# Kernel optimization log

Measured on AMD Instinct MI355X. Metric: run time of the kernel, lower is better.

The kernel has to match this reference:

```python
import jax, jax.numpy as jnp
import numpy as np

NUM_LAYERS = 2
D_MODEL = 64
D_INNER = 128   # expand * d_model
D_STATE = 128   # min(2*input_size, 256)
DT_RANK = 4     # ceil(d_model / 16)
D_CONV = 4
HIDDEN = 64


def _causal_dwconv(x, w, b):
    # x: [B, L, C], w: [C, K], b: [C]  -- causal depthwise conv (left pad K-1)
    K = w.shape[1]
    L = x.shape[1]
    xp = jnp.pad(x, ((0, 0), (K - 1, 0), (0, 0)))
    y = sum(xp[:, k:k + L, :] * w[:, k][None, None, :] for k in range(K))
    return y + b


def _selective_scan(u, delta, A, B, C, Dp):
    # u, delta: [b,L,d]; A: [d,n]; B, C: [b,L,n]; Dp: [d]
    dA = jnp.exp(jnp.einsum('bld,dn->lbdn', delta, A))          # [L,b,d,n]
    dBu = jnp.einsum('bld,bln,bld->lbdn', delta, B, u)           # [L,b,d,n]
    Ct = jnp.swapaxes(C, 0, 1)                                   # [L,b,n]

    def step(h, inp):
        dA_t, dBu_t, C_t = inp
        h = dA_t * h + dBu_t                                     # [b,d,n]
        y = jnp.einsum('bdn,bn->bd', h, C_t)
        return h, y

    h0 = jnp.zeros(dA.shape[1:], dA.dtype)
    _, ys = jax.lax.scan(step, h0, (dA, dBu, Ct))                # ys: [L,b,d]
    return jnp.swapaxes(ys, 0, 1) + u * Dp


def _mamba_layer(x, in_w, conv_w, conv_b, xproj_w, dt_w, dt_b, A_log, Dp, out_w):
    xz = x @ in_w.T                                              # [B,L,2*d_inner]
    xi, z = jnp.split(xz, 2, axis=-1)
    xi = jax.nn.silu(_causal_dwconv(xi, conv_w, conv_b))
    xdbl = xi @ xproj_w.T                                        # [B,L,dt_rank+2*d_state]
    delta = jax.nn.softplus(xdbl[..., :DT_RANK] @ dt_w.T + dt_b)
    Bm = xdbl[..., DT_RANK:DT_RANK + D_STATE]
    Cm = xdbl[..., DT_RANK + D_STATE:]
    A = -jnp.exp(A_log)
    y = _selective_scan(xi, delta, A, Bm, Cm, Dp)
    y = y * jax.nn.silu(z)
    return y @ out_w.T


def setup_inputs() -> dict:
    key = jax.random.key(0)
    ks = jax.random.split(key, 10)
    B, L = 4, 1024
    s = 0.05
    x = jax.random.normal(ks[0], (B, L, D_MODEL), dtype=jnp.float32)
    in_proj_w = jax.random.normal(ks[1], (NUM_LAYERS, 2 * D_INNER, D_MODEL)) * s
    conv_w = jax.random.normal(ks[2], (NUM_LAYERS, D_INNER, D_CONV)) * 0.2
    conv_b = jax.random.normal(ks[3], (NUM_LAYERS, D_INNER)) * 0.02
    x_proj_w = jax.random.normal(ks[4], (NUM_LAYERS, DT_RANK + 2 * D_STATE, D_INNER)) * s
    dt_w = jax.random.normal(ks[5], (NUM_LAYERS, D_INNER, DT_RANK)) * 0.1
    dt_b = jnp.full((NUM_LAYERS, D_INNER), -4.6, dtype=jnp.float32)  # softplus -> ~0.01
    # S4D-real init: A_log = log(1..d_state)
    A_log = jnp.log(jnp.broadcast_to(
        jnp.arange(1, D_STATE + 1, dtype=jnp.float32), (NUM_LAYERS, D_INNER, D_STATE)))
    D = jnp.ones((NUM_LAYERS, D_INNER), dtype=jnp.float32)
    out_proj_w = jax.random.normal(ks[6], (NUM_LAYERS, D_MODEL, D_INNER)) * s
    fc_w = jax.random.normal(ks[7], (HIDDEN, D_MODEL)) * s
    fc_b = jax.random.normal(ks[8], (HIDDEN,)) * 0.02
    return {"x": x, "in_proj_w": in_proj_w, "conv_w": conv_w, "conv_b": conv_b,
            "x_proj_w": x_proj_w, "dt_w": dt_w, "dt_b": dt_b, "A_log": A_log,
            "D": D, "out_proj_w": out_proj_w, "fc_w": fc_w, "fc_b": fc_b}


def reference(x, in_proj_w, conv_w, conv_b, x_proj_w, dt_w, dt_b, A_log, D, out_proj_w, fc_w, fc_b):
    h = x
    for l in range(NUM_LAYERS):
        h = _mamba_layer(h, in_proj_w[l], conv_w[l], conv_b[l], x_proj_w[l],
                         dt_w[l], dt_b[l], A_log[l], D[l], out_proj_w[l])
    return h @ fc_w.T + fc_b
```

## Files before the change

### kernel.cpp

```cpp
#include <hip/hip_runtime.h>
#include <hip/hip_bf16.h>

#define BB 4
#define LL 1024
#define DM 64
#define DI 128
#define DS 128
#define DTR 4
#define KC 4
#define RT 8
#define GRP 8
#define CS 128
#define NC 8
#define L2E 1.44269504f

#define XWT_OFF   0
#define INWT_OFF  65536
#define OWT_OFF   98304
#define CWT_OFF   114688
#define CB_OFF    115712
#define DTWT_OFF  115968
#define DTB_OFF   116992
#define XWDT_OFF  117248

__device__ __forceinline__ float bf2f(__hip_bfloat16 v) { return __bfloat162float(v); }
__device__ __forceinline__ float silu_f(float x) { return x / (1.f + __expf(-x)); }

__device__ __forceinline__ float ldf(const void* p, long i, unsigned bf) {
    return bf ? __bfloat162float(((const __hip_bfloat16*)p)[i]) : ((const float*)p)[i];
}

__device__ __forceinline__ void fma4(float4& acc, float s, const float4 w) {
    acc.x = fmaf(s, w.x, acc.x); acc.y = fmaf(s, w.y, acc.y);
    acc.z = fmaf(s, w.z, acc.z); acc.w = fmaf(s, w.w, acc.w);
}

__device__ __forceinline__ int permrb(int j) { return (j & 31) * 16 + (j >> 5); }

__device__ __forceinline__ void probe_flags(const void* dtb, const void* fcw,
                                            unsigned& bfe, unsigned& bfw) {
    unsigned w = *(const unsigned*)dtb;
    bfe = (w == 0xC093C093u) ? 1u : 0u;
    const unsigned* p = (const unsigned*)fcw;
    int cnt = 0;
    for (int i = 0; i < 32; ++i) {
        unsigned m = p[i] & 0x7FFFu;
        if (m >= 0x3000u && m < 0x4200u) cnt++;
    }
    bfw = (cnt >= 28) ? 1u : 0u;
}

__global__ __launch_bounds__(256) void k_prep(
        const void* __restrict__ inw, const void* __restrict__ xw,
        const void* __restrict__ ow, const void* __restrict__ cw,
        const void* __restrict__ cb, const void* __restrict__ dtw,
        const void* __restrict__ dtb, const void* __restrict__ fcw,
        unsigned* __restrict__ flags, float* __restrict__ WT) {
    unsigned bfe, bfw;
    probe_flags(dtb, fcw, bfe, bfw);
    int bid = blockIdx.x, tid = threadIdx.x;
    if (bid < 28) {
        const void* src; long soff; int srcK; float* dst; int dstN; int n0, k0;
        if (bid < 16) {
            int l = bid >> 3, kt = (bid >> 2) & 1, nt = bid & 3;
            src = xw; srcK = 128; soff = (long)l * 260 * 128 + 4 * 128;
            n0 = nt * 64; k0 = kt * 64; dst = WT + XWT_OFF + l * 32768; dstN = 256;
        } else if (bid < 24) {
            int b2 = bid - 16, l = b2 >> 2, nt = b2 & 3;
            src = inw; srcK = 64; soff = (long)l * 256 * 64;
            n0 = nt * 64; k0 = 0; dst = WT + INWT_OFF + l * 16384; dstN = 256;
        } else {
            int b2 = bid - 24, l = b2 >> 1, kt = b2 & 1;
            src = ow; srcK = 128; soff = (long)l * 64 * 128;
            n0 = 0; k0 = kt * 64; dst = WT + OWT_OFF + l * 8192; dstN = 64;
        }
        __shared__ float tile[64 * 65];
        for (int i = tid; i < 4096; i += 256) {
            int ln = i >> 6, lk = i & 63;
            tile[ln * 65 + lk] = ldf(src, soff + (long)(n0 + ln) * srcK + k0 + lk, bfw);
        }
        __syncthreads();
        for (int i = tid; i < 4096; i += 256) {
            int lk = i >> 6, ln = i & 63;
            dst[(long)(k0 + lk) * dstN + n0 + ln] = tile[ln * 65 + lk];
        }
    } else {
        if (tid == 0) { flags[0] = bfe; flags[1] = bfw; flags[2] = bfe & bfw; }
        for (int j = tid; j < 1024; j += 256) {
            int l = j >> 9, t = (j >> 7) & 3, d = j & 127;
            WT[CWT_OFF + j] = ldf(cw, (long)l * 512 + d * 4 + t, bfw);
        }
        for (int j = tid; j < 256; j += 256) WT[CB_OFF + j] = ldf(cb, j, bfw);
        for (int j = tid; j < 1024; j += 256) {
            int l = j >> 9, r = (j >> 7) & 3, d = j & 127;
            WT[DTWT_OFF + j] = ldf(dtw, (long)l * 512 + d * 4 + r, bfw);
        }
        for (int j = tid; j < 256; j += 256) WT[DTB_OFF + j] = ldf(dtb, j, bfe);
        for (int j = tid; j < 1024; j += 256) {
            int l = j >> 9, rem = j & 511;
            WT[XWDT_OFF + j] = ldf(xw, (long)l * 260 * 128 + rem, bfw);
        }
    }
}

__global__ __launch_bounds__(256) void k_inproj(
        const void* __restrict__ xin,
        const float* __restrict__ wt, const unsigned* __restrict__ flags,
        float* __restrict__ xzx, float* __restrict__ sz) {
    unsigned bfx = flags[0];
    int row0 = permrb(blockIdx.x) * RT;
    int tid = threadIdx.x, lane = tid & 63, g = tid >> 6;
    __shared__ float act[RT * DM];
    for (int i = tid; i < RT * DM; i += 256)
        act[i] = ldf(xin, (long)(row0 + (i >> 6)) * DM + (i & 63), bfx);
    __syncthreads();
    const float4* wt4 = (const float4*)wt;
    float4 acc[2];
    acc[0] = make_float4(0.f, 0.f, 0.f, 0.f);
    acc[1] = make_float4(0.f, 0.f, 0.f, 0.f);
#pragma unroll 8
    for (int k4 = 0; k4 < DM / 4; ++k4) {
        float4 w0 = wt4[(k4 * 4 + 0) * 64 + lane];
        float4 w1 = wt4[(k4 * 4 + 1) * 64 + lane];
        float4 w2 = wt4[(k4 * 4 + 2) * 64 + lane];
        float4 w3 = wt4[(k4 * 4 + 3) * 64 + lane];
#pragma unroll
        for (int r = 0; r < 2; ++r) {
            float4 av = *(const float4*)&act[(g * 2 + r) * DM + k4 * 4];
            fma4(acc[r], av.x, w0); fma4(acc[r], av.y, w1);
            fma4(acc[r], av.z, w2); fma4(acc[r], av.w, w3);
        }
    }
    int n0 = lane * 4;
#pragma unroll
    for (int r = 0; r < 2; ++r) {
        int row = row0 + g * 2 + r;
        if (n0 < DI) {
            *(float4*)&xzx[(size_t)row * DI + n0] = acc[r];
        } else {
            float4 v;
            v.x = silu_f(acc[r].x); v.y = silu_f(acc[r].y);
            v.z = silu_f(acc[r].z); v.w = silu_f(acc[r].w);
            *(float4*)&sz[(size_t)row * DI + (n0 - DI)] = v;
        }
    }
}

__global__ __launch_bounds__(256) void k_xproj(
        const float* __restrict__ xzx,
        const float* __restrict__ cwT, const float* __restrict__ cbF,
        const float* __restrict__ xwT, const float* __restrict__ xwdtF,
        const float* __restrict__ dtwT, const float* __restrict__ dtbF,
        float* __restrict__ xiw, float* __restrict__ dlt,
        float* __restrict__ Bm, float* __restrict__ Cm) {
    int row0 = permrb(blockIdx.x) * RT;
    int b = row0 >> 10, l0 = row0 & (LL - 1);
    int tid = threadIdx.x, lane = tid & 63, g = tid >> 6;
    __shared__ float xc[(RT + KC - 1) * DI];
    __shared__ float act[RT * DI];
    __shared__ float dtp[RT * DTR];
    for (int i = tid; i < (RT + KC - 1) * DI; i += 256) {
        int r = (i >> 7) - (KC - 1);
        int l = l0 + r;
        xc[i] = (l >= 0) ? xzx[((size_t)b * LL + l) * DI + (i & 127)] : 0.f;
    }
    __syncthreads();
    for (int i = tid; i < RT * DI; i += 256) {
        int r = i >> 7, d = i & 127;
        float a = cbF[d];
#pragma unroll
        for (int t = 0; t < KC; ++t) a = fmaf(xc[(r + t) * DI + d], cwT[t * DI + d], a);
        float v = silu_f(a);
        act[i] = v;
        xiw[(size_t)(row0 + r) * DI + d] = v;
    }
    __syncthreads();
    const float4* wt4 = (const float4*)xwT;
    float4 acc[2];
    acc[0] = make_float4(0.f, 0.f, 0.f, 0.f);
    acc[1] = make_float4(0.f, 0.f, 0.f, 0.f);
#pragma unroll 8
    for (int k4 = 0; k4 < DI / 4; ++k4) {
        float4 w0 = wt4[(k4 * 4 + 0) * 64 + lane];
        float4 w1 = wt4[(k4 * 4 + 1) * 64 + lane];
        float4 w2 = wt4[(k4 * 4 + 2) * 64 + lane];
        float4 w3 = wt4[(k4 * 4 + 3) * 64 + lane];
#pragma unroll
        for (int r = 0; r < 2; ++r) {
            float4 av = *(const float4*)&act[(g * 2 + r) * DI + k4 * 4];
            fma4(acc[r], av.x, w0); fma4(acc[r], av.y, w1);
            fma4(acc[r], av.z, w2); fma4(acc[r], av.w, w3);
        }
    }
    int n0 = lane * 4;
#pragma unroll
    for (int r = 0; r < 2; ++r) {
        int row = row0 + g * 2 + r;
        if (n0 < DS) *(float4*)&Bm[(size_t)row * DS + n0] = acc[r];
        else         *(float4*)&Cm[(size_t)row * DS + (n0 - DS)] = acc[r];
    }
    if (tid < RT * DTR) {
        int r = tid >> 2, i = tid & 3;
        float a = 0.f;
#pragma unroll
        for (int k4 = 0; k4 < DI / 4; ++k4) {
            float4 av = *(const float4*)&act[r * DI + k4 * 4];
            float4 wv = *(const float4*)&xwdtF[i * DI + k4 * 4];
            a = fmaf(av.x, wv.x, a); a = fmaf(av.y, wv.y, a);
            a = fmaf(av.z, wv.z, a); a = fmaf(av.w, wv.w, a);
        }
        dtp[tid] = a;
    }
    __syncthreads();
    if (tid < DI) {
        float dw0 = dtwT[0 * DI + tid], dw1 = dtwT[1 * DI + tid];
        float dw2 = dtwT[2 * DI + tid], dw3 = dtwT[3 * DI + tid];
        float bv = dtbF[tid];
#pragma unroll
        for (int r = 0; r < RT; ++r) {
            float a = bv;
            a = fmaf(dtp[r * 4 + 0], dw0, a);
            a = fmaf(dtp[r * 4 + 1], dw1, a);
            a = fmaf(dtp[r * 4 + 2], dw2, a);
            a = fmaf(dtp[r * 4 + 3], dw3, a);
            dlt[(size_t)(row0 + r) * DI + tid] = (a > 20.f) ? a : log1pf(__expf(a));
        }
    }
}

__global__ __launch_bounds__(256) void k_scanA(
        const float* __restrict__ dlt, const float* __restrict__ xiw,
        const float* __restrict__ Bm,
        const void* __restrict__ Alog, long aoff,
        const unsigned* __restrict__ flags,
        float* __restrict__ hend, float* __restrict__ S) {
    __shared__ float dsh[CS * 4];
    __shared__ float ush[CS * 4];
    int gid = blockIdx.x;
    int dg = gid / (BB * NC);
    int bc = gid % (BB * NC);
    int b = bc / NC, c = bc % NC;
    int d0 = dg * 4;
    int tid = threadIdx.x;
    int w = tid >> 6, t = tid & 63;
    int d = d0 + w;
    int c0 = c * CS;
    unsigned bfe = flags[0];
    float A0 = -L2E * __expf(ldf(Alog, aoff + (long)d * DS + 2 * t, bfe));
    float A1 = -L2E * __expf(ldf(Alog, aoff + (long)d * DS + 2 * t + 1, bfe));
    for (int i = tid; i < CS * 4; i += 256) {
        size_t src = ((size_t)b * LL + c0 + (i >> 2)) * DI + d0 + (i & 3);
        dsh[i] = dlt[src];
        ush[i] = xiw[src];
    }
    __syncthreads();
    const float2* Bg = (const float2*)(Bm + ((size_t)b * LL + c0) * DS) + t;
    float h0 = 0.f, h1v = 0.f, sumd = 0.f;
    for (int li = 0; li < CS; li += GRP) {
        float dl[GRP], ul[GRP], ea0[GRP], ea1[GRP];
        float2 Bv[GRP];
#pragma unroll
        for (int s = 0; s < GRP; ++s) {
            dl[s] = dsh[(li + s) * 4 + w];
            ul[s] = ush[(li + s) * 4 + w];
            Bv[s] = Bg[(size_t)(li + s) * (DS / 2)];
        }
#pragma unroll
        for (int s = 0; s < GRP; ++s) {
            ea0[s] = exp2f(dl[s] * A0);
            ea1[s] = exp2f(dl[s] * A1);
        }
#pragma unroll
        for (int s = 0; s < GRP; ++s) {
            float db = dl[s] * ul[s];
            h0  = fmaf(ea0[s], h0,  db * Bv[s].x);
            h1v = fmaf(ea1[s], h1v, db * Bv[s].y);
            sumd += dl[s];
        }
    }
    size_t hbase = (((size_t)b * DI + d) * NC + c) * DS;
    ((float2*)(hend + hbase))[t] = make_float2(h0, h1v);
    if (t == 0) S[((size_t)b * DI + d) * NC + c] = sumd;
}

__global__ __launch_bounds__(256) void k_scanC(
        const float* __restrict__ dlt, const float* __restrict__ xiw,
        const float* __restrict__ Bm, const float* __restrict__ Cm,
        const void* __restrict__ Alog, long aoff,
        const void* __restrict__ Dp, long doff,
        const unsigned* __restrict__ flags,
        const float* __restrict__ hend, const float* __restrict__ S,
        float* __restrict__ y) {
    __shared__ float dsh[CS * 4];
    __shared__ float ush[CS * 4];
    __shared__ float ysh[CS * 4];
    __shared__ float Wred[4 * 520];
    int gid = blockIdx.x;
    int dg = gid / (BB * NC);
    int bc = gid % (BB * NC);
    int b = bc / NC, c = bc % NC;
    int d0 = dg * 4;
    int tid = threadIdx.x;
    int w = tid >> 6, t = tid & 63;
    int d = d0 + w;
    int c0 = c * CS;
    unsigned bfe = flags[0];
    float A0 = -L2E * __expf(ldf(Alog, aoff + (long)d * DS + 2 * t, bfe));
    float A1 = -L2E * __expf(ldf(Alog, aoff + (long)d * DS + 2 * t + 1, bfe));
    float Dv = ldf(Dp, doff + d, bfe);
    for (int i = tid; i < CS * 4; i += 256) {
        size_t src = ((size_t)b * LL + c0 + (i >> 2)) * DI + d0 + (i & 3);
        dsh[i] = dlt[src];
        ush[i] = xiw[src];
    }
    __syncthreads();
    float h0 = 0.f, h1v = 0.f;
    const float2* hep = (const float2*)(hend + (((size_t)b * DI + d) * NC) * DS);
    const float* Sp = S + ((size_t)b * DI + d) * NC;
    for (int cc = 0; cc < c; ++cc) {
        float2 he = hep[(size_t)cc * (DS / 2) + t];
        float s = Sp[cc];
        h0  = fmaf(exp2f(A0 * s), h0,  he.x);
        h1v = fmaf(exp2f(A1 * s), h1v, he.y);
    }
    const float2* Bg = (const float2*)(Bm + ((size_t)b * LL + c0) * DS) + t;
    const float2* Cg = (const float2*)(Cm + ((size_t)b * LL + c0) * DS) + t;
    float* Wl = Wred + w * 520;
    int rbase = (t >> 3) * 65 + (t & 7) * 8;
    for (int li = 0; li < CS; li += GRP) {
        float dl[GRP], ul[GRP], ea0[GRP], ea1[GRP], cv[GRP];
        float2 Bv[GRP], Cv[GRP];
#pragma unroll
        for (int s = 0; s < GRP; ++s) {
            dl[s] = dsh[(li + s) * 4 + w];
            ul[s] = ush[(li + s) * 4 + w];
            Bv[s] = Bg[(size_t)(li + s) * (DS / 2)];
            Cv[s] = Cg[(size_t)(li + s) * (DS / 2)];
        }
#pragma unroll
        for (int s = 0; s < GRP; ++s) {
            ea0[s] = exp2f(dl[s] * A0);
            ea1[s] = exp2f(dl[s] * A1);
        }
#pragma unroll
        for (int s = 0; s < GRP; ++s) {
            float db = dl[s] * ul[s];
            h0  = fmaf(ea0[s], h0,  db * Bv[s].x);
            h1v = fmaf(ea1[s], h1v, db * Bv[s].y);
            cv[s] = fmaf(h0, Cv[s].x, h1v * Cv[s].y);
        }
#pragma unroll
        for (int s = 0; s < GRP; ++s) Wl[s * 65 + t] = cv[s];
        float pt = 0.f;
#pragma unroll
        for (int j = 0; j < 8; ++j) pt += Wl[rbase + j];
        pt += __shfl_xor(pt, 1, 64);
        pt += __shfl_xor(pt, 2, 64);
        pt += __shfl_xor(pt, 4, 64);
        if ((t & 7) == 0) {
            int l = li + (t >> 3);
            ysh[l * 4 + w] = pt + ush[l * 4 + w] * Dv;
        }
    }
    __syncthreads();
    for (int i = tid; i < CS * 4; i += 256)
        y[((size_t)b * LL + c0 + (i >> 2)) * DI + d0 + (i & 3)] = ysh[i];
}

__global__ __launch_bounds__(256) void k_mid(
        const float* __restrict__ y, float* __restrict__ sz,
        const float* __restrict__ owT, const float* __restrict__ inwT,
        float* __restrict__ xzx) {
    int row0 = permrb(blockIdx.x) * RT;
    int tid = threadIdx.x, lane = tid & 63, g = tid >> 6;
    __shared__ float act[RT * DI];
    __shared__ float hsh[RT * DM];
    for (int i = tid; i < RT * DI; i += 256) {
        size_t idx = (size_t)(row0 + (i >> 7)) * DI + (i & 127);
        act[i] = y[idx] * sz[idx];
    }
    __syncthreads();
    {
        float acc[2] = {0.f, 0.f};
#pragma unroll 8
        for (int k4 = 0; k4 < DI / 4; ++k4) {
            float w0 = owT[(k4 * 4 + 0) * DM + lane];
            float w1 = owT[(k4 * 4 + 1) * DM + lane];
            float w2 = owT[(k4 * 4 + 2) * DM + lane];
            float w3 = owT[(k4 * 4 + 3) * DM + lane];
#pragma unroll
            for (int r = 0; r < 2; ++r) {
                float4 av = *(const float4*)&act[(g * 2 + r) * DI + k4 * 4];
                acc[r] = fmaf(av.x, w0, acc[r]); acc[r] = fmaf(av.y, w1, acc[r]);
                acc[r] = fmaf(av.z, w2, acc[r]); acc[r] = fmaf(av.w, w3, acc[r]);
            }
        }
#pragma unroll
        for (int r = 0; r < 2; ++r) hsh[(g * 2 + r) * DM + lane] = acc[r];
    }
    __syncthreads();
    {
        const float4* wt4 = (const float4*)inwT;
        float4 acc[2];
        acc[0] = make_float4(0.f, 0.f, 0.f, 0.f);
        acc[1] = make_float4(0.f, 0.f, 0.f, 0.f);
#pragma unroll 8
        for (int k4 = 0; k4 < DM / 4; ++k4) {
            float4 w0 = wt4[(k4 * 4 + 0) * 64 + lane];
            float4 w1 = wt4[(k4 * 4 + 1) * 64 + lane];
            float4 w2 = wt4[(k4 * 4 + 2) * 64 + lane];
            float4 w3 = wt4[(k4 * 4 + 3) * 64 + lane];
#pragma unroll
            for (int r = 0; r < 2; ++r) {
                float4 av = *(const float4*)&hsh[(g * 2 + r) * DM + k4 * 4];
                fma4(acc[r], av.x, w0); fma4(acc[r], av.y, w1);
                fma4(acc[r], av.z, w2); fma4(acc[r], av.w, w3);
            }
        }
        int n0 = lane * 4;
#pragma unroll
        for (int r = 0; r < 2; ++r) {
            int row = row0 + g * 2 + r;
            if (n0 < DI) {
                *(float4*)&xzx[(size_t)row * DI + n0] = acc[r];
            } else {
                float4 v;
                v.x = silu_f(acc[r].x); v.y = silu_f(acc[r].y);
                v.z = silu_f(acc[r].z); v.w = silu_f(acc[r].w);
                *(float4*)&sz[(size_t)row * DI + (n0 - DI)] = v;
            }
        }
    }
}

__global__ __launch_bounds__(256) void k_back(
        const float* __restrict__ y, const float* __restrict__ sz,
        const void* __restrict__ ow, long owoff,
        const void* __restrict__ fw, const void* __restrict__ fb,
        const unsigned* __restrict__ flags, void* __restrict__ out) {
    unsigned bfw = flags[1], obf = flags[2];
    int row0 = permrb(blockIdx.x) * RT;
    int tid = threadIdx.x, n = tid & 63, g = tid >> 6;
    __shared__ float owsh[DI * 65];
    __shared__ float fwsh[DM * 65];
    __shared__ float act[RT * DI];
    __shared__ float hsh[RT * DM];
    for (int i = tid; i < DM * DI; i += 256) {
        int nn = i >> 7, k = i & 127;
        owsh[k * 65 + nn] = ldf(ow, owoff + i, bfw);
    }
    for (int i = tid; i < DM * DM; i += 256) {
        int nn = i >> 6, k = i & 63;
        fwsh[k * 65 + nn] = ldf(fw, i, bfw);
    }
    for (int i = tid; i < RT * DI; i += 256) {
        size_t idx = (size_t)(row0 + (i >> 7)) * DI + (i & 127);
        act[i] = y[idx] * sz[idx];
    }
    __syncthreads();
    {
        float acc[2] = {0.f, 0.f};
#pragma unroll 8
        for (int k4 = 0; k4 < DI / 4; ++k4) {
            float w0 = owsh[(k4 * 4 + 0) * 65 + n];
            float w1 = owsh[(k4 * 4 + 1) * 65 + n];
            float w2 = owsh[(k4 * 4 + 2) * 65 + n];
            float w3 = owsh[(k4 * 4 + 3) * 65 + n];
#pragma unroll
            for (int r = 0; r < 2; ++r) {
                float4 av = *(const float4*)&act[(g * 2 + r) * DI + k4 * 4];
                acc[r] = fmaf(av.x, w0, acc[r]); acc[r] = fmaf(av.y, w1, acc[r]);
                acc[r] = fmaf(av.z, w2, acc[r]); acc[r] = fmaf(av.w, w3, acc[r]);
            }
        }
#pragma unroll
        for (int r = 0; r < 2; ++r) hsh[(g * 2 + r) * DM + n] = acc[r];
    }
    __syncthreads();
    {
        float bv = ldf(fb, n, bfw);
        float acc[2] = {bv, bv};
#pragma unroll 8
        for (int k4 = 0; k4 < DM / 4; ++k4) {
            float w0 = fwsh[(k4 * 4 + 0) * 65 + n];
            float w1 = fwsh[(k4 * 4 + 1) * 65 + n];
            float w2 = fwsh[(k4 * 4 + 2) * 65 + n];
            float w3 = fwsh[(k4 * 4 + 3) * 65 + n];
#pragma unroll
            for (int r = 0; r < 2; ++r) {
                float4 av = *(const float4*)&hsh[(g * 2 + r) * DM + k4 * 4];
                acc[r] = fmaf(av.x, w0, acc[r]); acc[r] = fmaf(av.y, w1, acc[r]);
                acc[r] = fmaf(av.z, w2, acc[r]); acc[r] = fmaf(av.w, w3, acc[r]);
            }
        }
#pragma unroll
        for (int r = 0; r < 2; ++r) {
            size_t idx = (size_t)(row0 + g * 2 + r) * DM + n;
            if (obf) ((__hip_bfloat16*)out)[idx] = __float2bfloat16(acc[r]);
            else     ((float*)out)[idx] = acc[r];
        }
    }
}

extern "C" void kernel_launch(void* const* d_in, const int* in_sizes, int n_in,
                              void* d_out, int out_size, void* d_ws, size_t ws_size,
                              hipStream_t stream) {
    const void* x    = d_in[0];
    const void* inw  = d_in[1];
    const void* cw   = d_in[2];
    const void* cb   = d_in[3];
    const void* xw   = d_in[4];
    const void* dtw  = d_in[5];
    const void* dtb  = d_in[6];
    const void* Alog = d_in[7];
    const void* Dp   = d_in[8];
    const void* ow   = d_in[9];
    const void* fcw  = d_in[10];
    const void* fcb  = d_in[11];

    const size_t NBL = (size_t)BB * LL;
    const int GB = (int)(NBL / RT);
    unsigned* flags = (unsigned*)d_ws;
    float* base = (float*)d_ws + 64;
    float* sz   = base;
    float* xiw  = sz + 524288;
    float* dlt  = xiw + 524288;
    float* Bmw  = dlt + 524288;
    float* Cmw  = Bmw + 524288;
    float* yw   = Cmw + 524288;
    float* hend = yw + 524288;
    float* S    = hend + 524288;
    float* xzx  = S + 4096;
    float* WT   = (float*)d_out;

    k_prep<<<29, 256, 0, stream>>>(inw, xw, ow, cw, cb, dtw, dtb, fcw, flags, WT);

    k_inproj<<<GB, 256, 0, stream>>>(x, WT + INWT_OFF, flags, xzx, sz);
    k_xproj<<<GB, 256, 0, stream>>>(xzx,
                                    WT + CWT_OFF, WT + CB_OFF,
                                    WT + XWT_OFF, WT + XWDT_OFF,
                                    WT + DTWT_OFF, WT + DTB_OFF,
                                    xiw, dlt, Bmw, Cmw);
    k_scanA<<<32 * BB * NC, 256, 0, stream>>>(dlt, xiw, Bmw, Alog, 0, flags, hend, S);
    k_scanC<<<32 * BB * NC, 256, 0, stream>>>(dlt, xiw, Bmw, Cmw, Alog, 0,
                                              Dp, 0, flags, hend, S, yw);
    k_mid<<<GB, 256, 0, stream>>>(yw, sz, WT + OWT_OFF, WT + INWT_OFF + 16384, xzx);
    k_xproj<<<GB, 256, 0, stream>>>(xzx,
                                    WT + CWT_OFF + 512, WT + CB_OFF + 128,
                                    WT + XWT_OFF + 32768, WT + XWDT_OFF + 512,
                                    WT + DTWT_OFF + 512, WT + DTB_OFF + 128,
                                    xiw, dlt, Bmw, Cmw);
    k_scanA<<<32 * BB * NC, 256, 0, stream>>>(dlt, xiw, Bmw, Alog, (long)DI * DS, flags, hend, S);
    k_scanC<<<32 * BB * NC, 256, 0, stream>>>(dlt, xiw, Bmw, Cmw, Alog, (long)DI * DS,
                                              Dp, DI, flags, hend, S, yw);
    k_back<<<GB, 256, 0, stream>>>(yw, sz, ow, (long)DM * DI, fcw, fcb, flags, d_out);
}
```

Measured before the change: 299.1 us.

## Fuse chunked scan passes into one kernel with inter-block flag handoff

Merges the two-pass chunked selective scan (chunk-end state pass, then output pass) into one kernel. Each block scans its chunk from a zero state, publishes its end state and delta sum, then waits on release/acquire flags from earlier chunks. It adds their carried-in contribution using a prefix sum of delta over the chunk. This removes one kernel launch and the duplicate recomputation of the local recurrence per layer. The price is spin-waiting that assumes earlier chunks' blocks are resident or already done, plus an extra exp pass for the carry term.

```diff
diff --git a/kernel.cpp b/kernel.cpp
--- a/kernel.cpp
+++ b/kernel.cpp
@@ -228,14 +228,20 @@
     }
 }
 
-__global__ __launch_bounds__(256) void k_scanA(
+__global__ __launch_bounds__(256) void k_scanF2(
         const float* __restrict__ dlt, const float* __restrict__ xiw,
-        const float* __restrict__ Bm,
+        const float* __restrict__ Bm, const float* __restrict__ Cm,
         const void* __restrict__ Alog, long aoff,
+        const void* __restrict__ Dp, long doff,
         const unsigned* __restrict__ flags,
-        float* __restrict__ hend, float* __restrict__ S) {
+        float* __restrict__ hend, float* __restrict__ S,
+        unsigned* __restrict__ flagArr, unsigned magic,
+        float* __restrict__ y) {
     __shared__ float dsh[CS * 4];
-    __shared__ float ush[CS * 4];
+    __shared__ float dush[CS * 4];
+    __shared__ float cdsh[CS * 4];
+    __shared__ float ysh[CS * 4];
+    __shared__ float Wred[4 * 520];
     int gid = blockIdx.x;
     int dg = gid / (BB * NC);
     int bc = gid % (BB * NC);
@@ -250,90 +256,43 @@
     float A1 = -L2E * __expf(ldf(Alog, aoff + (long)d * DS + 2 * t + 1, bfe));
     for (int i = tid; i < CS * 4; i += 256) {
         size_t src = ((size_t)b * LL + c0 + (i >> 2)) * DI + d0 + (i & 3);
-        dsh[i] = dlt[src];
-        ush[i] = xiw[src];
-    }
-    __syncthreads();
-    const float2* Bg = (const float2*)(Bm + ((size_t)b * LL + c0) * DS) + t;
-    float h0 = 0.f, h1v = 0.f, sumd = 0.f;
-    for (int li = 0; li < CS; li += GRP) {
-        float dl[GRP], ul[GRP], ea0[GRP], ea1[GRP];
-        float2 Bv[GRP];
-#pragma unroll
-        for (int s = 0; s < GRP; ++s) {
-            dl[s] = dsh[(li + s) * 4 + w];
-            ul[s] = ush[(li + s) * 4 + w];
-            Bv[s] = Bg[(size_t)(li + s) * (DS / 2)];
-        }
-#pragma unroll
-        for (int s = 0; s < GRP; ++s) {
-            ea0[s] = exp2f(dl[s] * A0);
-            ea1[s] = exp2f(dl[s] * A1);
-        }
-#pragma unroll
-        for (int s = 0; s < GRP; ++s) {
-            float db = dl[s] * ul[s];
-            h0  = fmaf(ea0[s], h0,  db * Bv[s].x);
-            h1v = fmaf(ea1[s], h1v, db * Bv[s].y);
-            sumd += dl[s];
-        }
-    }
-    size_t hbase = (((size_t)b * DI + d) * NC + c) * DS;
-    ((float2*)(hend + hbase))[t] = make_float2(h0, h1v);
-    if (t == 0) S[((size_t)b * DI + d) * NC + c] = sumd;
-}
-
-__global__ __launch_bounds__(256) void k_scanC(
-        const float* __restrict__ dlt, const float* __restrict__ xiw,
-        const float* __restrict__ Bm, const float* __restrict__ Cm,
-        const void* __restrict__ Alog, long aoff,
-        const void* __restrict__ Dp, long doff,
-        const unsigned* __restrict__ flags,
-        const float* __restrict__ hend, const float* __restrict__ S,
-        float* __restrict__ y) {
-    __shared__ float dsh[CS * 4];
-    __shared__ float ush[CS * 4];
-    __shared__ float ysh[CS * 4];
-    __shared__ float Wred[4 * 520];
-    int gid = blockIdx.x;
-    int dg = gid / (BB * NC);
-    int bc = gid % (BB * NC);
-    int b = bc / NC, c = bc % NC;
-    int d0 = dg * 4;
-    int tid = threadIdx.x;
-    int w = tid >> 6, t = tid & 63;
-    int d = d0 + w;
-    int c0 = c * CS;
-    unsigned bfe = flags[0];
-    float A0 = -L2E * __expf(ldf(Alog, aoff + (long)d * DS + 2 * t, bfe));
-    float A1 = -L2E * __expf(ldf(Alog, aoff + (long)d * DS + 2 * t + 1, bfe));
-    float Dv = ldf(Dp, doff + d, bfe);
-    for (int i = tid; i < CS * 4; i += 256) {
-        size_t src = ((size_t)b * LL + c0 + (i >> 2)) * DI + d0 + (i & 3);
-        dsh[i] = dlt[src];
-        ush[i] = xiw[src];
-    }
-    __syncthreads();
-    float h0 = 0.f, h1v = 0.f;
-    const float2* hep = (const float2*)(hend + (((size_t)b * DI + d) * NC) * DS);
-    const float* Sp = S + ((size_t)b * DI + d) * NC;
-    for (int cc = 0; cc < c; ++cc) {
-        float2 he = hep[(size_t)cc * (DS / 2) + t];
-        float s = Sp[cc];
-        h0  = fmaf(exp2f(A0 * s), h0,  he.x);
-        h1v = fmaf(exp2f(A1 * s), h1v, he.y);
+        float dl = dlt[src];
+        float ul = xiw[src];
+        dsh[i] = dl;
+        dush[i] = dl * ul;
+        ysh[i] = ul * ldf(Dp, doff + d0 + (i & 3), bfe);
+    }
+    __syncthreads();
+    {
+        float a = dsh[t * 4 + w];
+        float bb2 = dsh[(64 + t) * 4 + w];
+#pragma unroll
+        for (int off = 1; off < 64; off <<= 1) {
+            float n = __shfl(a, t - off, 64);
+            if (t >= off) a += n;
+        }
+        float T1 = __shfl(a, 63, 64);
+#pragma unroll
+        for (int off = 1; off < 64; off <<= 1) {
+            float n = __shfl(bb2, t - off, 64);
+            if (t >= off) bb2 += n;
+        }
+        bb2 += T1;
+        cdsh[t * 4 + w] = a;
+        cdsh[(64 + t) * 4 + w] = bb2;
     }
     const float2* Bg = (const float2*)(Bm + ((size_t)b * LL + c0) * DS) + t;
     const float2* Cg = (const float2*)(Cm + ((size_t)b * LL + c0) * DS) + t;
     float* Wl = Wred + w * 520;
     int rbase = (t >> 3) * 65 + (t & 7) * 8;
+    float h0 = 0.f, h1v = 0.f;
     for (int li = 0; li < CS; li += GRP) {
-        float dl[GRP], ul[GRP], ea0[GRP], ea1[GRP], cv[GRP];
+        float dl[GRP], du[GRP], ea0[GRP], ea1[GRP], cv[GRP];
         float2 Bv[GRP], Cv[GRP];
 #pragma unroll
         for (int s = 0; s < GRP; ++s) {
             dl[s] = dsh[(li + s) * 4 + w];
-            ul[s] = ush[(li + s) * 4 + w];
+            du[s] = dush[(li + s) * 4 + w];
             Bv[s] = Bg[(size_t)(li + s) * (DS / 2)];
             Cv[s] = Cg[(size_t)(li + s) * (DS / 2)];
         }
@@ -344,9 +303,8 @@
         }
 #pragma unroll
         for (int s = 0; s < GRP; ++s) {
-            float db = dl[s] * ul[s];
-            h0  = fmaf(ea0[s], h0,  db * Bv[s].x);
-            h1v = fmaf(ea1[s], h1v, db * Bv[s].y);
+            h0  = fmaf(ea0[s], h0,  du[s] * Bv[s].x);
+            h1v = fmaf(ea1[s], h1v, du[s] * Bv[s].y);
             cv[s] = fmaf(h0, Cv[s].x, h1v * Cv[s].y);
         }
 #pragma unroll
@@ -359,7 +317,64 @@
         pt += __shfl_xor(pt, 4, 64);
         if ((t & 7) == 0) {
             int l = li + (t >> 3);
-            ysh[l * 4 + w] = pt + ush[l * 4 + w] * Dv;
+            ysh[l * 4 + w] += pt;
+        }
+    }
+    if (c < NC - 1) {
+        size_t hbase = (((size_t)b * DI + d) * NC + c) * DS;
+        ((float2*)(hend + hbase))[t] = make_float2(h0, h1v);
+        if (t == 0) S[((size_t)b * DI + d) * NC + c] = cdsh[127 * 4 + w];
+        __threadfence();
+        __syncthreads();
+        if (tid == 0)
+            __hip_atomic_store(&flagArr[(b * NC + c) * 32 + dg], magic,
+                               __ATOMIC_RELEASE, __HIP_MEMORY_SCOPE_AGENT);
+    }
+    if (c > 0) {
+        if (tid < c) {
+            while (__hip_atomic_load(&flagArr[(b * NC + tid) * 32 + dg],
+                                     __ATOMIC_ACQUIRE, __HIP_MEMORY_SCOPE_AGENT) != magic) {
+                __builtin_amdgcn_s_sleep(1);
+            }
+        }
+        __syncthreads();
+        float hi0 = 0.f, hi1 = 0.f;
+        const float2* hep = (const float2*)(hend + (((size_t)b * DI + d) * NC) * DS);
+        const float* Sp = S + ((size_t)b * DI + d) * NC;
+        for (int cc = 0; cc < c; ++cc) {
+            float2 he = hep[(size_t)cc * (DS / 2) + t];
+            float s = Sp[cc];
+            hi0 = fmaf(exp2f(A0 * s), hi0, he.x);
+            hi1 = fmaf(exp2f(A1 * s), hi1, he.y);
+        }
+        for (int li = 0; li < CS; li += GRP) {
+            float cd[GRP], ea0[GRP], ea1[GRP], cv[GRP];
+            float2 Cv[GRP];
+#pragma unroll
+            for (int s = 0; s < GRP; ++s) {
+                cd[s] = cdsh[(li + s) * 4 + w];
+                Cv[s] = Cg[(size_t)(li + s) * (DS / 2)];
+            }
+#pragma unroll
+            for (int s = 0; s < GRP; ++s) {
+                ea0[s] = exp2f(cd[s] * A0);
+                ea1[s] = exp2f(cd[s] * A1);
+            }
+#pragma unroll
+            for (int s = 0; s < GRP; ++s)
+                cv[s] = fmaf(hi0 * ea0[s], Cv[s].x, hi1 * ea1[s] * Cv[s].y);
+#pragma unroll
+            for (int s = 0; s < GRP; ++s) Wl[s * 65 + t] = cv[s];
+            float pt = 0.f;
+#pragma unroll
+            for (int j = 0; j < 8; ++j) pt += Wl[rbase + j];
+            pt += __shfl_xor(pt, 1, 64);
+            pt += __shfl_xor(pt, 2, 64);
+            pt += __shfl_xor(pt, 4, 64);
+            if ((t & 7) == 0) {
+                int l = li + (t >> 3);
+                ysh[l * 4 + w] += pt;
+            }
         }
     }
     __syncthreads();
@@ -531,6 +546,7 @@
     float* hend = yw + 524288;
     float* S    = hend + 524288;
     float* xzx  = S + 4096;
+    unsigned* flagArr = (unsigned*)(xzx + 524288);
     float* WT   = (float*)d_out;
 
     k_prep<<<29, 256, 0, stream>>>(inw, xw, ow, cw, cb, dtw, dtb, fcw, flags, WT);
@@ -541,17 +557,17 @@
                                     WT + XWT_OFF, WT + XWDT_OFF,
                                     WT + DTWT_OFF, WT + DTB_OFF,
                                     xiw, dlt, Bmw, Cmw);
-    k_scanA<<<32 * BB * NC, 256, 0, stream>>>(dlt, xiw, Bmw, Alog, 0, flags, hend, S);
-    k_scanC<<<32 * BB * NC, 256, 0, stream>>>(dlt, xiw, Bmw, Cmw, Alog, 0,
-                                              Dp, 0, flags, hend, S, yw);
+    k_scanF2<<<32 * BB * NC, 256, 0, stream>>>(dlt, xiw, Bmw, Cmw, Alog, 0,
+                                               Dp, 0, flags, hend, S,
+                                               flagArr, 0x5CA6F00Du, yw);
     k_mid<<<GB, 256, 0, stream>>>(yw, sz, WT + OWT_OFF, WT + INWT_OFF + 16384, xzx);
     k_xproj<<<GB, 256, 0, stream>>>(xzx,
                                     WT + CWT_OFF + 512, WT + CB_OFF + 128,
                                     WT + XWT_OFF + 32768, WT + XWDT_OFF + 512,
                                     WT + DTWT_OFF + 512, WT + DTB_OFF + 128,
                                     xiw, dlt, Bmw, Cmw);
-    k_scanA<<<32 * BB * NC, 256, 0, stream>>>(dlt, xiw, Bmw, Alog, (long)DI * DS, flags, hend, S);
-    k_scanC<<<32 * BB * NC, 256, 0, stream>>>(dlt, xiw, Bmw, Cmw, Alog, (long)DI * DS,
-                                              Dp, DI, flags, hend, S, yw);
+    k_scanF2<<<32 * BB * NC, 256, 0, stream>>>(dlt, xiw, Bmw, Cmw, Alog, (long)DI * DS,
+                                               Dp, DI, flags, hend, S,
+                                               flagArr, 0x5CA6F00Eu, yw);
     k_back<<<GB, 256, 0, stream>>>(yw, sz, ow, (long)DM * DI, fcw, fcb, flags, d_out);
 }
```

Result: slower. 545.5 us (+82.4%).
